# Kernel optimization log

Hardware: AMD Instinct MI355X
Metric: run time of the kernel (lower is better)

The kernel has to match this reference:

```python
import jax, jax.numpy as jnp
import numpy as np

EPS = 1e-7        # min norm to avoid div-by-zero
BALL_EPS = 1e-5   # Poincare-ball boundary clip


def _norm(x):
    return jnp.maximum(jnp.linalg.norm(x, axis=-1, keepdims=True), EPS)


def expmap0(u, c):
    sc = jnp.sqrt(c)
    n = _norm(u)
    return jnp.tanh(sc * n) * u / (sc * n)


def logmap0(p, c):
    sc = jnp.sqrt(c)
    n = _norm(p)
    return jnp.arctanh(jnp.minimum(sc * n, 1.0 - BALL_EPS)) * p / (sc * n)


def proj(x, c):
    # project onto the ball of radius (1-eps)/sqrt(c)
    n = _norm(x)
    maxn = (1.0 - BALL_EPS) / jnp.sqrt(c)
    return jnp.where(n > maxn, x * (maxn / n), x)


def mobius_matvec(W, x, c):
    # Mobius matrix-vector multiply on the Poincare ball
    sc = jnp.sqrt(c)
    xn = _norm(x)                       # [N,1]
    mx = x @ W                          # [N,D]
    mxn = _norm(mx)
    t = jnp.tanh((mxn / xn) * jnp.arctanh(jnp.minimum(sc * xn, 1.0 - BALL_EPS)))
    return t * mx / (sc * mxn)


def spmm(rows, cols, vals, x):
    # sparse(adj) @ x, adjacency in COO form
    return jax.ops.segment_sum(vals[:, None] * x[cols], rows, num_segments=x.shape[0])


def hgc_layer(x, rows, cols, vals, W, c, c_lin):
    t = logmap0(x, c)                               # to tangent space at origin
    h = proj(mobius_matvec(W, t, c_lin), c_lin)     # LinearHyperbolic (c=1.0, no activation)
    s = spmm(rows, cols, vals, h)                   # HyperbolicAggregation: adj @ h
    agg = proj(expmap0(s, c), c)
    a = jax.nn.relu(logmap0(agg, c))                # ActivationHyperbolic (relu, c_in=c_out=c)
    return proj(expmap0(a, c), c)


def setup_inputs() -> dict:
    key = jax.random.key(0)
    ks = jax.random.split(key, 7)
    N, D, E = 10000, 1433, 100000
    x = jax.random.normal(ks[0], (N, D), jnp.float32) * 0.1  # keep points off the boundary
    rows = jax.random.randint(ks[1], (E,), 0, N)
    cols = jax.random.randint(ks[2], (E,), 0, N)
    vals = jax.random.uniform(ks[3], (E,), jnp.float32) / 10.0  # ~normalized adjacency weights
    scale = 1.0 / np.sqrt(D)
    W0 = jax.random.normal(ks[4], (D, D), jnp.float32) * scale
    W1 = jax.random.normal(ks[5], (D, D), jnp.float32) * scale
    W2 = jax.random.normal(ks[6], (D, D), jnp.float32) * scale
    return {"x": x, "W0": W0, "W1": W1, "W2": W2, "vals": vals, "rows": rows, "cols": cols}


def reference(x, W0, W1, W2, vals, rows, cols):
    c = jnp.float32(0.4)       # c_map == c0 for every layer in the source
    c_lin = jnp.float32(1.0)   # LinearHyperbolic hard-coded c
    h = expmap0(x, c)
    for W in (W0, W1, W2):
        h = hgc_layer(h, rows, cols, vals, W, c, c_lin)
    return h
```

## Files before the change

### kernel.cpp

```cpp
#include <hip/hip_runtime.h>

typedef unsigned short u16;
typedef unsigned int   u32;

#define M_ROWS 10000
#define D_DIM  1433
#define KPAD   1472
#define NPAD   1536
#define MPAD   10240
#define N_EDGE 100000
#define HPAD   1440
#define HP32   720
#define NKT    23
#define EPS    1e-7f
#define BEPS   1e-5f
#define SC     0.6324555320336759f

typedef __bf16 bf16x8 __attribute__((ext_vector_type(8)));
typedef float  f32x4  __attribute__((ext_vector_type(4)));
typedef u32    u32x4  __attribute__((ext_vector_type(4)));

__device__ __forceinline__ u16 f2bf(float f) {
  union { float f; unsigned u; } v; v.f = f;
  unsigned r = v.u + 0x7FFFu + ((v.u >> 16) & 1u);
  return (u16)(r >> 16);
}
__device__ __forceinline__ u32 pack2bf(float lo, float hi) {
  return (u32)f2bf(lo) | ((u32)f2bf(hi) << 16);
}
__device__ __forceinline__ float bflo(u32 u) { return __uint_as_float(u << 16); }
__device__ __forceinline__ float bfhi(u32 u) { return __uint_as_float(u & 0xFFFF0000u); }

__device__ __forceinline__ float atanh_f(float y) {
  return 0.5f * logf((1.f + y) / (1.f - y));
}

__device__ __forceinline__ void gl_lds16(const u16* g, u16* l) {
  __builtin_amdgcn_global_load_lds((const __attribute__((address_space(1))) void*)(const void*)g,
                                   (__attribute__((address_space(3))) void*)(void*)l,
                                   16, 0, 0);
}

#define BAR() asm volatile("s_barrier" ::: "memory")

__global__ __launch_bounds__(512, 1) void gemm256(
    const u16* __restrict__ A,
    const u16* __restrict__ B,
    u16* __restrict__ C,
    float* __restrict__ nrm)
{
  __shared__ u16 lds[2][2][256 * 64];

  const int tid  = threadIdx.x;
  const int lane = tid & 63;
  const int w    = tid >> 6;
  const int wr   = w >> 2;
  const int wc   = w & 3;

  const int flat = blockIdx.x;
  const int wgid = (flat & 7) * 30 + (flat >> 3);
  const int gy = wgid % 6;
  const int gx = wgid / 6;
  const long arow0 = (long)gx * 256;
  const long brow0 = (long)gy * 256;

  f32x4 acc[8][4] = {};

  const int sr8 = lane >> 3;
  const int scb = ((lane & 7) << 4) ^ (sr8 << 4);
  const int l15 = lane & 15;
  const int khi = (lane >> 4) << 4;

  auto STG_B = [&](int b, int kt) {
    const long k0 = (long)kt * 64 + (scb >> 1);
#pragma unroll
    for (int l = 0; l < 4; ++l) {
      const int r   = l * 64 + w * 8 + sr8;
      const int dst = l * 4096 + w * 512;
      gl_lds16(B + (brow0 + r) * KPAD + k0, &lds[b][1][dst]);
    }
  };
  auto STG_A = [&](int b, int kt, int sel) {
    const long k0 = (long)kt * 64 + (scb >> 1);
#pragma unroll
    for (int li = 0; li < 2; ++li) {
      const int l   = sel + 2 * li;
      const int r   = l * 64 + w * 8 + sr8;
      const int dst = l * 4096 + w * 512;
      gl_lds16(A + (arow0 + r) * KPAD + k0, &lds[b][0][dst]);
    }
  };

  STG_B(0, 0); STG_A(0, 0, 0); STG_A(0, 0, 1);
  asm volatile("s_waitcnt vmcnt(0)" ::: "memory");
  BAR();

  for (int kt = 0; kt < NKT; ++kt) {
    const int b = kt & 1;
    const bool pf = (kt + 1 < NKT);

    bf16x8 b0[4], b1[4], a0[4], a1[4];
#pragma unroll
    for (int ni = 0; ni < 4; ++ni) {
      const int row = wc * 64 + ni * 16 + l15;
      const int kb0 = (khi) ^ ((row & 7) << 4);
      const int kb1 = (64 + khi) ^ ((row & 7) << 4);
      b0[ni] = *(const bf16x8*)&lds[b][1][row * 64 + (kb0 >> 1)];
      b1[ni] = *(const bf16x8*)&lds[b][1][row * 64 + (kb1 >> 1)];
    }
#pragma unroll
    for (int ml = 0; ml < 4; ++ml) {
      const int row = wr * 128 + ml * 16 + l15;
      const int kb0 = (khi) ^ ((row & 7) << 4);
      const int kb1 = (64 + khi) ^ ((row & 7) << 4);
      a0[ml] = *(const bf16x8*)&lds[b][0][row * 64 + (kb0 >> 1)];
      a1[ml] = *(const bf16x8*)&lds[b][0][row * 64 + (kb1 >> 1)];
    }
    if (pf) { STG_B(b ^ 1, kt + 1); STG_A(b ^ 1, kt + 1, 0); }
    __builtin_amdgcn_s_setprio(1);
#pragma unroll
    for (int ml = 0; ml < 4; ++ml)
#pragma unroll
      for (int ni = 0; ni < 4; ++ni)
        acc[ml][ni] = __builtin_amdgcn_mfma_f32_16x16x32_bf16(a0[ml], b0[ni], acc[ml][ni], 0, 0, 0);
#pragma unroll
    for (int ml = 0; ml < 4; ++ml)
#pragma unroll
      for (int ni = 0; ni < 4; ++ni)
        acc[ml][ni] = __builtin_amdgcn_mfma_f32_16x16x32_bf16(a1[ml], b1[ni], acc[ml][ni], 0, 0, 0);
    __builtin_amdgcn_s_setprio(0);
    if (pf) asm volatile("s_waitcnt vmcnt(6)" ::: "memory");
    else    asm volatile("s_waitcnt vmcnt(0)" ::: "memory");
    BAR();

    bf16x8 c0[4], c1[4];
#pragma unroll
    for (int ml = 0; ml < 4; ++ml) {
      const int row = wr * 128 + (4 + ml) * 16 + l15;
      const int kb0 = (khi) ^ ((row & 7) << 4);
      const int kb1 = (64 + khi) ^ ((row & 7) << 4);
      c0[ml] = *(const bf16x8*)&lds[b][0][row * 64 + (kb0 >> 1)];
      c1[ml] = *(const bf16x8*)&lds[b][0][row * 64 + (kb1 >> 1)];
    }
    if (pf) STG_A(b ^ 1, kt + 1, 1);
    __builtin_amdgcn_s_setprio(1);
#pragma unroll
    for (int ml = 0; ml < 4; ++ml)
#pragma unroll
      for (int ni = 0; ni < 4; ++ni)
        acc[4 + ml][ni] = __builtin_amdgcn_mfma_f32_16x16x32_bf16(c0[ml], b0[ni], acc[4 + ml][ni], 0, 0, 0);
#pragma unroll
    for (int ml = 0; ml < 4; ++ml)
#pragma unroll
      for (int ni = 0; ni < 4; ++ni)
        acc[4 + ml][ni] = __builtin_amdgcn_mfma_f32_16x16x32_bf16(c1[ml], b1[ni], acc[4 + ml][ni], 0, 0, 0);
    __builtin_amdgcn_s_setprio(0);
    if (pf) asm volatile("s_waitcnt vmcnt(2)" ::: "memory");
    BAR();
  }

  const int orw = (lane >> 4) * 4;
  const int ocl = lane & 15;

#pragma unroll
  for (int mi = 0; mi < 8; ++mi)
#pragma unroll
    for (int r = 0; r < 4; ++r) {
      float s = 0.f;
#pragma unroll
      for (int ni = 0; ni < 4; ++ni) {
        const long j = brow0 + wc * 64 + ni * 16 + ocl;
        const float v = acc[mi][ni][r];
        s += (j < D_DIM) ? v * v : 0.f;
      }
      s += __shfl_xor(s, 1, 64);
      s += __shfl_xor(s, 2, 64);
      s += __shfl_xor(s, 4, 64);
      s += __shfl_xor(s, 8, 64);
      if ((lane & 15) == 0)
        atomicAdd(&nrm[arow0 + wr * 128 + mi * 16 + orw + r], s);
    }

#pragma unroll
  for (int mi = 0; mi < 8; ++mi) {
    const long i0 = arow0 + wr * 128 + mi * 16 + orw;
    if (i0 >= M_ROWS) continue;
#pragma unroll
    for (int ni = 0; ni < 4; ++ni) {
      const long j = brow0 + wc * 64 + ni * 16 + ocl;
      if (j >= HPAD) continue;
#pragma unroll
      for (int r = 0; r < 4; ++r) {
        const long i = i0 + r;
        if (i < M_ROWS) C[i * HPAD + j] = (j < D_DIM) ? f2bf(acc[mi][ni][r]) : (u16)0;
      }
    }
  }
}

template<int NW>
__device__ __forceinline__ float2 block_reduce2(float a, float b) {
  __shared__ float sa[NW], sb[NW];
#pragma unroll
  for (int off = 32; off > 0; off >>= 1) {
    a += __shfl_down(a, off, 64);
    b += __shfl_down(b, off, 64);
  }
  const int tid = threadIdx.x;
  if ((tid & 63) == 0) { sa[tid >> 6] = a; sb[tid >> 6] = b; }
  __syncthreads();
  float ra = 0.f, rb = 0.f;
#pragma unroll
  for (int i = 0; i < NW; ++i) { ra += sa[i]; rb += sb[i]; }
  __syncthreads();
  return make_float2(ra, rb);
}

__global__ __launch_bounds__(256) void pre_k(const float* __restrict__ x,
                                             u16* __restrict__ t,
                                             float* __restrict__ xn) {
  const long i = blockIdx.x;
  const int tid = threadIdx.x;
  u16* trow = t + i * KPAD;
  if (i >= M_ROWS) {
#pragma unroll
    for (int jj = 0; jj < 6; ++jj) { int j = tid + jj * 256; if (j < KPAD) trow[j] = 0; }
    return;
  }
  const float* xr = x + i * D_DIM;
  float v[6]; float s2 = 0.f;
#pragma unroll
  for (int jj = 0; jj < 6; ++jj) {
    int j = tid + jj * 256;
    v[jj] = (j < D_DIM) ? xr[j] : 0.f;
    s2 += v[jj] * v[jj];
  }
  s2 = block_reduce2<4>(s2, 0.f).x;
  const float nx_t = sqrtf(s2);
  const float nx   = fmaxf(nx_t, EPS);
  const float al   = tanhf(SC * nx) / (SC * nx);
  const float n1   = fmaxf(al * nx_t, EPS);
  const float be   = atanh_f(fminf(SC * n1, 1.f - BEPS)) / (SC * n1);
  const float sca  = al * be;
  if (tid == 0) xn[i] = fmaxf(sca * nx_t, EPS);
#pragma unroll
  for (int jj = 0; jj < 6; ++jj) {
    int j = tid + jj * 256;
    if (j < KPAD) trow[j] = (j < D_DIM) ? f2bf(sca * v[jj]) : (u16)0;
  }
}

__global__ void zero_f(float* p, int n) {
  int i = blockIdx.x * 256 + threadIdx.x;
  if (i < n) p[i] = 0.f;
}

__global__ void fold_k(const int* __restrict__ ecol, const float* __restrict__ eval,
                       const float* __restrict__ nrm, const float* __restrict__ xn,
                       u32* __restrict__ pe, int E) {
  const int e = blockIdx.x * 256 + threadIdx.x;
  if (e >= E) return;
  const int c = ecol[e];
  const float realn = sqrtf(nrm[c]);
  const float mxn   = fmaxf(realn, EPS);
  const float xi    = xn[c];
  const float tf    = tanhf((mxn / xi) * atanh_f(fminf(xi, 1.f - BEPS)));
  float S = tf / mxn;
  const float hn = fmaxf(S * realn, EPS);
  const float maxn = 1.f - BEPS;
  if (hn > maxn) S *= maxn / hn;
  pe[e] = ((u32)c << 16) | (u32)f2bf(eval[e] * S);
}

__global__ __launch_bounds__(256) void spmm_post(const int* __restrict__ rp,
                                                 const u32* __restrict__ pe,
                                                 const u32* __restrict__ mxp,
                                                 u16* __restrict__ t,
                                                 float* __restrict__ xn,
                                                 float* __restrict__ out,
                                                 const int last) {
  const long r = blockIdx.x;
  const int tid = threadIdx.x;
  if (r >= M_ROWS) {
    if (!last && tid < 184) {
      u32* trow32 = (u32*)(t + r * KPAD);
#pragma unroll
      for (int k = 0; k < 4; ++k) trow32[4 * tid + k] = 0u;
    }
    return;
  }
  const bool act = tid < 180;
  const long boff = 4 * tid;
  float a[8] = {0.f, 0.f, 0.f, 0.f, 0.f, 0.f, 0.f, 0.f};
  const int e0 = rp[r], e1 = rp[r + 1];
  for (int e = e0; e < e1; e += 12) {
    u32 pp[12]; float w[12];
#pragma unroll
    for (int j = 0; j < 12; ++j) {
      const int ee = e + j;
      const int ec = (ee < e1) ? ee : (e1 - 1);
      pp[j] = pe[ec];
      w[j]  = (ee < e1) ? bflo(pp[j]) : 0.f;
    }
    if (act) {
      u32x4 q[12];
#pragma unroll
      for (int j = 0; j < 12; ++j)
        q[j] = *(const u32x4*)&mxp[(long)(pp[j] >> 16) * HP32 + boff];
#pragma unroll
      for (int j = 0; j < 12; ++j) {
#pragma unroll
        for (int k = 0; k < 4; ++k) {
          a[2 * k]     += w[j] * bflo(q[j][k]);
          a[2 * k + 1] += w[j] * bfhi(q[j][k]);
        }
      }
    }
  }
  float s2 = 0.f, s2p = 0.f;
#pragma unroll
  for (int k = 0; k < 8; ++k) {
    const int col = 8 * tid + k;
    const float v = (act && col < D_DIM) ? a[k] : 0.f;
    a[k] = v;
    s2 += v * v;
    const float p = fmaxf(v, 0.f);
    s2p += p * p;
  }
  const float2 red = block_reduce2<4>(s2, s2p);
  const float ns_t  = sqrtf(red.x);
  const float nsp_t = sqrtf(red.y);
  const float maxn = (1.f - BEPS) / SC;
  const float ns = fmaxf(ns_t, EPS);
  const float al = tanhf(SC * ns) / (SC * ns);
  const float n1 = fmaxf(al * ns_t, EPS);
  const float be = (n1 > maxn) ? (maxn / n1) : 1.f;
  const float n2 = fmaxf(be * al * ns_t, EPS);
  const float lam = atanh_f(fminf(SC * n2, 1.f - BEPS)) / (SC * n2);
  const float g = lam * be * al;
  const float na_t = g * nsp_t;
  const float n3 = fmaxf(na_t, EPS);
  const float mu = tanhf(SC * n3) / (SC * n3);
  const float n4 = fmaxf(mu * na_t, EPS);
  const float nu = (n4 > maxn) ? (maxn / n4) : 1.f;
  const float T = nu * mu * g;
  if (last) {
    if (act) {
      float* orow = out + r * (long)D_DIM;
#pragma unroll
      for (int k = 0; k < 8; ++k) {
        const int col = 8 * tid + k;
        if (col < D_DIM) orow[col] = T * fmaxf(a[k], 0.f);
      }
    }
  } else {
    const float nh_t = T * nsp_t;
    const float n5 = fmaxf(nh_t, EPS);
    const float kap = atanh_f(fminf(SC * n5, 1.f - BEPS)) / (SC * n5);
    const float F = kap * T;
    if (tid == 0) xn[r] = fmaxf(F * nsp_t, EPS);
    u32* trow32 = (u32*)(t + r * KPAD);
    if (act) {
#pragma unroll
      for (int k = 0; k < 4; ++k)
        trow32[4 * tid + k] = pack2bf(F * fmaxf(a[2 * k], 0.f), F * fmaxf(a[2 * k + 1], 0.f));
    } else if (tid < 184) {
#pragma unroll
      for (int k = 0; k < 4; ++k) trow32[4 * tid + k] = 0u;
    }
  }
}

__global__ void wt_conv(const float* __restrict__ W, u16* __restrict__ Wt) {
  __shared__ float tile[32][33];
  const int kb = blockIdx.x * 32, nb = blockIdx.y * 32;
  const int tx = threadIdx.x, ty = threadIdx.y;
#pragma unroll
  for (int r = 0; r < 32; r += 8) {
    const int k = kb + ty + r, n = nb + tx;
    tile[ty + r][tx] = (k < D_DIM && n < D_DIM) ? W[(long)k * D_DIM + n] : 0.f;
  }
  __syncthreads();
#pragma unroll
  for (int r = 0; r < 32; r += 8) {
    const int n = nb + ty + r, k = kb + tx;
    if (n < NPAD && k < KPAD) Wt[(long)n * KPAD + k] = f2bf(tile[tx][ty + r]);
  }
}

__global__ void zero_int(int* p, int n) {
  int i = blockIdx.x * 256 + threadIdx.x;
  if (i < n) p[i] = 0;
}
__global__ void hist_k(const int* __restrict__ rows, int* __restrict__ counts, int E) {
  int e = blockIdx.x * 256 + threadIdx.x;
  if (e < E) atomicAdd(&counts[rows[e]], 1);
}
__global__ __launch_bounds__(1024) void scan_rp(const int* __restrict__ counts,
                                                int* __restrict__ rp, int n) {
  __shared__ int swv[16];
  __shared__ int carry_s;
  const int tid  = threadIdx.x;
  const int lane = tid & 63;
  const int wid  = tid >> 6;
  if (tid == 0) { carry_s = 0; rp[0] = 0; }
  __syncthreads();
  for (int base = 0; base < n; base += 1024) {
    const int i = base + tid;
    int v = (i < n) ? counts[i] : 0;
#pragma unroll
    for (int off = 1; off < 64; off <<= 1) {
      const int tv = __shfl_up(v, off, 64);
      if (lane >= off) v += tv;
    }
    if (lane == 63) swv[wid] = v;
    __syncthreads();
    if (wid == 0) {
      int s = (lane < 16) ? swv[lane] : 0;
#pragma unroll
      for (int off = 1; off < 16; off <<= 1) {
        const int tv = __shfl_up(s, off, 64);
        if (lane >= off) s += tv;
      }
      if (lane < 16) swv[lane] = s;
    }
    __syncthreads();
    const int wpfx  = (wid > 0) ? swv[wid - 1] : 0;
    const int carry = carry_s;
    if (i < n) rp[i + 1] = carry + wpfx + v;
    __syncthreads();
    if (tid == 1023) carry_s = carry + swv[15];
    __syncthreads();
  }
}
__global__ void scatter_k(const int* __restrict__ rows, const int* __restrict__ cols,
                          const float* __restrict__ vals, const int* __restrict__ rp,
                          int* __restrict__ cursor, int* __restrict__ ecol,
                          float* __restrict__ eval, int E) {
  int e = blockIdx.x * 256 + threadIdx.x;
  if (e < E) {
    const int r = rows[e];
    const int pos = rp[r] + atomicAdd(&cursor[r], 1);
    ecol[pos] = cols[e];
    eval[pos] = vals[e];
  }
}

extern "C" void kernel_launch(void* const* d_in, const int* in_sizes, int n_in,
                              void* d_out, int out_size, void* d_ws, size_t ws_size,
                              hipStream_t stream) {
  (void)in_sizes; (void)n_in; (void)out_size; (void)ws_size;
  const float* x    = (const float*)d_in[0];
  const float* W[3] = {(const float*)d_in[1], (const float*)d_in[2], (const float*)d_in[3]};
  const float* vals = (const float*)d_in[4];
  const int*   rows = (const int*)d_in[5];
  const int*   cols = (const int*)d_in[6];
  float* out = (float*)d_out;

  char* base = (char*)d_ws;
  size_t off = 0;
  auto take = [&](size_t bytes) {
    void* q = base + off;
    off = (off + bytes + 255) & ~(size_t)255;
    return q;
  };
  u16*   t    = (u16*)take((size_t)MPAD * KPAD * 2);
  u16*   Wt   = (u16*)take((size_t)NPAD * KPAD * 2);
  u16*   mx   = (u16*)take((size_t)M_ROWS * HPAD * 2);
  float* nrm3 = (float*)take((size_t)3 * MPAD * 4);
  float* xn   = (float*)take((size_t)M_ROWS * 4);
  int*   cnt  = (int*)take((size_t)M_ROWS * 2 * 4);
  int*   rp   = (int*)take((size_t)(M_ROWS + 1) * 4);
  int*   ecol = (int*)take((size_t)N_EDGE * 4);
  float* eval = (float*)take((size_t)N_EDGE * 4);
  u32*   pe   = (u32*)take((size_t)N_EDGE * 4);

  zero_int<<<(2 * M_ROWS + 255) / 256, 256, 0, stream>>>(cnt, 2 * M_ROWS);
  hist_k<<<(N_EDGE + 255) / 256, 256, 0, stream>>>(rows, cnt, N_EDGE);
  scan_rp<<<1, 1024, 0, stream>>>(cnt, rp, M_ROWS);
  scatter_k<<<(N_EDGE + 255) / 256, 256, 0, stream>>>(rows, cols, vals, rp,
                                                      cnt + M_ROWS, ecol, eval, N_EDGE);
  zero_f<<<(3 * MPAD + 255) / 256, 256, 0, stream>>>(nrm3, 3 * MPAD);

  pre_k<<<MPAD, 256, 0, stream>>>(x, t, xn);

  for (int L = 0; L < 3; ++L) {
    float* nrm = nrm3 + (size_t)L * MPAD;
    wt_conv<<<dim3(46, 48), dim3(32, 8), 0, stream>>>(W[L], Wt);
    gemm256<<<240, 512, 0, stream>>>(t, Wt, mx, nrm);
    fold_k<<<(N_EDGE + 255) / 256, 256, 0, stream>>>(ecol, eval, nrm, xn, pe, N_EDGE);
    spmm_post<<<MPAD, 256, 0, stream>>>(rp, pe, (const u32*)mx, t, xn, out, (L == 2) ? 1 : 0);
  }
}
```

Measured before the change: 361.1 us.

## Use 4-wave GEMM workgroups with 128x128 per-wave tiles

The GEMM workgroup goes from 8 waves in a 2x4 grid to 4 waves in a 2x2 grid. Each wave now computes a 128x128 output tile with 8x8 MFMA accumulators, which raises reuse of operand fragments read from LDS. The global-to-LDS staging loops and vmcnt wait counts are adjusted for the larger per-thread load count. In exchange, each SIMD runs only one wave, leaving less latency hiding, and register pressure rises sharply, which risks spilling or poorer overlap.

```diff
diff --git a/kernel.cpp b/kernel.cpp
--- a/kernel.cpp
+++ b/kernel.cpp
@@ -43,7 +43,7 @@
 
 #define BAR() asm volatile("s_barrier" ::: "memory")
 
-__global__ __launch_bounds__(512, 1) void gemm256(
+__global__ __launch_bounds__(256, 1) void gemm256(
     const u16* __restrict__ A,
     const u16* __restrict__ B,
     u16* __restrict__ C,
@@ -54,8 +54,8 @@
   const int tid  = threadIdx.x;
   const int lane = tid & 63;
   const int w    = tid >> 6;
-  const int wr   = w >> 2;
-  const int wc   = w & 3;
+  const int wr   = w >> 1;
+  const int wc   = w & 1;
 
   const int flat = blockIdx.x;
   const int wgid = (flat & 7) * 30 + (flat >> 3);
@@ -64,7 +64,7 @@
   const long arow0 = (long)gx * 256;
   const long brow0 = (long)gy * 256;
 
-  f32x4 acc[8][4] = {};
+  f32x4 acc[8][8] = {};
 
   const int sr8 = lane >> 3;
   const int scb = ((lane & 7) << 4) ^ (sr8 << 4);
@@ -74,88 +74,88 @@
   auto STG_B = [&](int b, int kt) {
     const long k0 = (long)kt * 64 + (scb >> 1);
 #pragma unroll
-    for (int l = 0; l < 4; ++l) {
-      const int r   = l * 64 + w * 8 + sr8;
-      const int dst = l * 4096 + w * 512;
+    for (int l = 0; l < 8; ++l) {
+      const int r   = l * 32 + w * 8 + sr8;
+      const int dst = l * 2048 + w * 512;
       gl_lds16(B + (brow0 + r) * KPAD + k0, &lds[b][1][dst]);
     }
   };
   auto STG_A = [&](int b, int kt, int sel) {
     const long k0 = (long)kt * 64 + (scb >> 1);
 #pragma unroll
-    for (int li = 0; li < 2; ++li) {
-      const int l   = sel + 2 * li;
-      const int r   = l * 64 + w * 8 + sr8;
-      const int dst = l * 4096 + w * 512;
+    for (int g = 0; g < 4; ++g) {
+      const int l   = (g >> 1) * 4 + sel * 2 + (g & 1);
+      const int r   = l * 32 + w * 8 + sr8;
+      const int dst = l * 2048 + w * 512;
       gl_lds16(A + (arow0 + r) * KPAD + k0, &lds[b][0][dst]);
     }
   };
 
   STG_B(0, 0); STG_A(0, 0, 0); STG_A(0, 0, 1);
-  asm volatile("s_waitcnt vmcnt(0)" ::: "memory");
+  asm volatile("s_waitcnt vmcnt(4)" ::: "memory");
   BAR();
 
   for (int kt = 0; kt < NKT; ++kt) {
     const int b = kt & 1;
     const bool pf = (kt + 1 < NKT);
 
-    bf16x8 b0[4], b1[4], a0[4], a1[4];
-#pragma unroll
-    for (int ni = 0; ni < 4; ++ni) {
-      const int row = wc * 64 + ni * 16 + l15;
+    bf16x8 b0[8], b1[8], a0[4], a1[4];
+#pragma unroll
+    for (int ni = 0; ni < 8; ++ni) {
+      const int row = wc * 128 + ni * 16 + l15;
       const int kb0 = (khi) ^ ((row & 7) << 4);
       const int kb1 = (64 + khi) ^ ((row & 7) << 4);
       b0[ni] = *(const bf16x8*)&lds[b][1][row * 64 + (kb0 >> 1)];
       b1[ni] = *(const bf16x8*)&lds[b][1][row * 64 + (kb1 >> 1)];
     }
 #pragma unroll
-    for (int ml = 0; ml < 4; ++ml) {
-      const int row = wr * 128 + ml * 16 + l15;
+    for (int mi = 0; mi < 4; ++mi) {
+      const int row = wr * 128 + mi * 16 + l15;
       const int kb0 = (khi) ^ ((row & 7) << 4);
       const int kb1 = (64 + khi) ^ ((row & 7) << 4);
-      a0[ml] = *(const bf16x8*)&lds[b][0][row * 64 + (kb0 >> 1)];
-      a1[ml] = *(const bf16x8*)&lds[b][0][row * 64 + (kb1 >> 1)];
+      a0[mi] = *(const bf16x8*)&lds[b][0][row * 64 + (kb0 >> 1)];
+      a1[mi] = *(const bf16x8*)&lds[b][0][row * 64 + (kb1 >> 1)];
     }
     if (pf) { STG_B(b ^ 1, kt + 1); STG_A(b ^ 1, kt + 1, 0); }
     __builtin_amdgcn_s_setprio(1);
 #pragma unroll
-    for (int ml = 0; ml < 4; ++ml)
-#pragma unroll
-      for (int ni = 0; ni < 4; ++ni)
-        acc[ml][ni] = __builtin_amdgcn_mfma_f32_16x16x32_bf16(a0[ml], b0[ni], acc[ml][ni], 0, 0, 0);
-#pragma unroll
-    for (int ml = 0; ml < 4; ++ml)
-#pragma unroll
-      for (int ni = 0; ni < 4; ++ni)
-        acc[ml][ni] = __builtin_amdgcn_mfma_f32_16x16x32_bf16(a1[ml], b1[ni], acc[ml][ni], 0, 0, 0);
+    for (int mi = 0; mi < 4; ++mi)
+#pragma unroll
+      for (int ni = 0; ni < 8; ++ni)
+        acc[mi][ni] = __builtin_amdgcn_mfma_f32_16x16x32_bf16(a0[mi], b0[ni], acc[mi][ni], 0, 0, 0);
+#pragma unroll
+    for (int mi = 0; mi < 4; ++mi)
+#pragma unroll
+      for (int ni = 0; ni < 8; ++ni)
+        acc[mi][ni] = __builtin_amdgcn_mfma_f32_16x16x32_bf16(a1[mi], b1[ni], acc[mi][ni], 0, 0, 0);
     __builtin_amdgcn_s_setprio(0);
-    if (pf) asm volatile("s_waitcnt vmcnt(6)" ::: "memory");
+    if (pf) asm volatile("s_waitcnt vmcnt(12)" ::: "memory");
     else    asm volatile("s_waitcnt vmcnt(0)" ::: "memory");
     BAR();
 
     bf16x8 c0[4], c1[4];
 #pragma unroll
-    for (int ml = 0; ml < 4; ++ml) {
-      const int row = wr * 128 + (4 + ml) * 16 + l15;
+    for (int mi = 0; mi < 4; ++mi) {
+      const int row = wr * 128 + (4 + mi) * 16 + l15;
       const int kb0 = (khi) ^ ((row & 7) << 4);
       const int kb1 = (64 + khi) ^ ((row & 7) << 4);
-      c0[ml] = *(const bf16x8*)&lds[b][0][row * 64 + (kb0 >> 1)];
-      c1[ml] = *(const bf16x8*)&lds[b][0][row * 64 + (kb1 >> 1)];
+      c0[mi] = *(const bf16x8*)&lds[b][0][row * 64 + (kb0 >> 1)];
+      c1[mi] = *(const bf16x8*)&lds[b][0][row * 64 + (kb1 >> 1)];
     }
     if (pf) STG_A(b ^ 1, kt + 1, 1);
     __builtin_amdgcn_s_setprio(1);
 #pragma unroll
-    for (int ml = 0; ml < 4; ++ml)
-#pragma unroll
-      for (int ni = 0; ni < 4; ++ni)
-        acc[4 + ml][ni] = __builtin_amdgcn_mfma_f32_16x16x32_bf16(c0[ml], b0[ni], acc[4 + ml][ni], 0, 0, 0);
-#pragma unroll
-    for (int ml = 0; ml < 4; ++ml)
-#pragma unroll
-      for (int ni = 0; ni < 4; ++ni)
-        acc[4 + ml][ni] = __builtin_amdgcn_mfma_f32_16x16x32_bf16(c1[ml], b1[ni], acc[4 + ml][ni], 0, 0, 0);
+    for (int mi = 0; mi < 4; ++mi)
+#pragma unroll
+      for (int ni = 0; ni < 8; ++ni)
+        acc[4 + mi][ni] = __builtin_amdgcn_mfma_f32_16x16x32_bf16(c0[mi], b0[ni], acc[4 + mi][ni], 0, 0, 0);
+#pragma unroll
+    for (int mi = 0; mi < 4; ++mi)
+#pragma unroll
+      for (int ni = 0; ni < 8; ++ni)
+        acc[4 + mi][ni] = __builtin_amdgcn_mfma_f32_16x16x32_bf16(c1[mi], b1[ni], acc[4 + mi][ni], 0, 0, 0);
     __builtin_amdgcn_s_setprio(0);
-    if (pf) asm volatile("s_waitcnt vmcnt(2)" ::: "memory");
+    if (pf) asm volatile("s_waitcnt vmcnt(4)" ::: "memory");
     BAR();
   }
 
@@ -168,8 +168,8 @@
     for (int r = 0; r < 4; ++r) {
       float s = 0.f;
 #pragma unroll
-      for (int ni = 0; ni < 4; ++ni) {
-        const long j = brow0 + wc * 64 + ni * 16 + ocl;
+      for (int ni = 0; ni < 8; ++ni) {
+        const long j = brow0 + wc * 128 + ni * 16 + ocl;
         const float v = acc[mi][ni][r];
         s += (j < D_DIM) ? v * v : 0.f;
       }
@@ -186,8 +186,8 @@
     const long i0 = arow0 + wr * 128 + mi * 16 + orw;
     if (i0 >= M_ROWS) continue;
 #pragma unroll
-    for (int ni = 0; ni < 4; ++ni) {
-      const long j = brow0 + wc * 64 + ni * 16 + ocl;
+    for (int ni = 0; ni < 8; ++ni) {
+      const long j = brow0 + wc * 128 + ni * 16 + ocl;
       if (j >= HPAD) continue;
 #pragma unroll
       for (int r = 0; r < 4; ++r) {
@@ -487,7 +487,7 @@
   for (int L = 0; L < 3; ++L) {
     float* nrm = nrm3 + (size_t)L * MPAD;
     wt_conv<<<dim3(46, 48), dim3(32, 8), 0, stream>>>(W[L], Wt);
-    gemm256<<<240, 512, 0, stream>>>(t, Wt, mx, nrm);
+    gemm256<<<240, 256, 0, stream>>>(t, Wt, mx, nrm);
     fold_k<<<(N_EDGE + 255) / 256, 256, 0, stream>>>(ecol, eval, nrm, xn, pe, N_EDGE);
     spmm_post<<<MPAD, 256, 0, stream>>>(rp, pe, (const u32*)mx, t, xn, out, (L == 2) ? 1 : 0);
   }
```

New measurement: 395.7 us. 9.6% more time.
